# Kernel tuning notes

Measured on AMD Instinct MI355X. Metric: run time of the kernel, lower is better.

## Reference

```python
import jax, jax.numpy as jnp
import numpy as np

A = 9          # num anchors per location
C = 256        # feature channels
H = W = 32     # feature map size
B = 1          # batch (module's squeeze_-based NMS implies batch=1)
N = A * H * W  # total proposals
IOU_THR = 0.9
EPS = 1e-5     # BatchNorm eps
NEG_SLOPE = 0.01  # LeakyReLU default


def setup_inputs() -> dict:
    key = jax.random.key(0)
    ks = jax.random.split(key, 8)
    inp = {
        "x": jax.random.normal(ks[0], (B, C, H, W), dtype=jnp.float32),
        "anchors": jax.random.uniform(ks[1], (A, 4), dtype=jnp.float32),
        # depthwise 3x3 conv (groups=C): torch weight shape [C,1,3,3]
        "dw_w": jax.random.normal(ks[2], (C, 1, 3, 3), dtype=jnp.float32) * 0.05,
        # pointwise 1x1 conv [C_out, C_in]
        "pw_w": jax.random.normal(ks[3], (C, C), dtype=jnp.float32) * 0.05,
        "bn1_gamma": jnp.ones((C,), jnp.float32),
        "bn1_beta": jnp.zeros((C,), jnp.float32),
        "bn1_mean": jnp.zeros((C,), jnp.float32),
        "bn1_var": jnp.ones((C,), jnp.float32),
        # anchors_conv: 1x1 conv 256 -> 4A, BN, ReLU6
        "anc_w": jax.random.normal(ks[4], (4 * A, C), dtype=jnp.float32) * 0.05,
        "anc_gamma": jnp.ones((4 * A,), jnp.float32),
        "anc_beta": jnp.zeros((4 * A,), jnp.float32),
        "anc_mean": jnp.zeros((4 * A,), jnp.float32),
        "anc_var": jnp.ones((4 * A,), jnp.float32),
        # objectness_conv: 1x1 conv 256 -> A, BN, Sigmoid
        "obj_w": jax.random.normal(ks[5], (A, C), dtype=jnp.float32) * 0.05,
        "obj_gamma": jnp.ones((A,), jnp.float32),
        "obj_beta": jnp.zeros((A,), jnp.float32),
        "obj_mean": jnp.zeros((A,), jnp.float32),
        "obj_var": jnp.ones((A,), jnp.float32),
    }
    return inp


def _bn(h, gamma, beta, mean, var):
    # inference-mode BatchNorm2d over channel dim 1 of [B,C,H,W]
    inv = jax.lax.rsqrt(var + EPS)
    return (h - mean[None, :, None, None]) * (inv * gamma)[None, :, None, None] + beta[None, :, None, None]


def _nms_keep(boxes, scores, thr):
    # greedy NMS (torchvision semantics, boxes as x1,y1,x2,y2) -> bool keep mask in original order
    order = jnp.argsort(-scores)
    b = boxes[order]  # [N,4] sorted by score desc
    x1, y1, x2, y2 = b[:, 0], b[:, 1], b[:, 2], b[:, 3]
    areas = (x2 - x1) * (y2 - y1)
    ix1 = jnp.maximum(x1[:, None], x1[None, :])
    iy1 = jnp.maximum(y1[:, None], y1[None, :])
    ix2 = jnp.minimum(x2[:, None], x2[None, :])
    iy2 = jnp.minimum(y2[:, None], y2[None, :])
    inter = jnp.clip(ix2 - ix1, 0.0) * jnp.clip(iy2 - iy1, 0.0)
    iou = inter / (areas[:, None] + areas[None, :] - inter)
    idx = jnp.arange(boxes.shape[0])

    def body(i, keep):
        sup = (iou[i] > thr) & (idx > i) & keep[i]
        return keep & ~sup

    keep_sorted = jax.lax.fori_loop(0, boxes.shape[0], body, jnp.ones((boxes.shape[0],), bool))
    return jnp.zeros((boxes.shape[0],), bool).at[order].set(keep_sorted)


def reference(x, anchors, dw_w, pw_w, bn1_gamma, bn1_beta, bn1_mean, bn1_var,
              anc_w, anc_gamma, anc_beta, anc_mean, anc_var,
              obj_w, obj_gamma, obj_beta, obj_mean, obj_var):
    batch = x.shape[0]
    hw = x.shape[2] * x.shape[3]
    # DepthSeparableConv2d: depthwise 3x3 (groups=C) + pointwise 1x1
    h = jax.lax.conv_general_dilated(
        x, dw_w, window_strides=(1, 1), padding=((1, 1), (1, 1)),
        dimension_numbers=("NCHW", "OIHW", "NCHW"), feature_group_count=C)
    h = jnp.einsum("bchw,oc->bohw", h, pw_w)
    h = jax.nn.leaky_relu(_bn(h, bn1_gamma, bn1_beta, bn1_mean, bn1_var), NEG_SLOPE)
    # heads
    anc = jnp.einsum("bchw,oc->bohw", h, anc_w)
    anc = jnp.clip(_bn(anc, anc_gamma, anc_beta, anc_mean, anc_var), 0.0, 6.0)  # ReLU6
    obj = jnp.einsum("bchw,oc->bohw", h, obj_w)
    obj = jax.nn.sigmoid(_bn(obj, obj_gamma, obj_beta, obj_mean, obj_var))
    # anchor decode
    corr = anc.reshape(batch, A, 4, hw)              # [B,A,4,HW]
    anch = anchors.reshape(1, A, 4, 1)
    pos = corr[:, :, :2, :] + anch[:, :, :2, :]
    size = jnp.exp(corr[:, :, 2:, :]) * anch[:, :, 2:, :]
    corrected = jnp.concatenate([pos, size], axis=2)  # [B,A,4,HW]
    boxes = corrected.transpose(0, 2, 1, 3).reshape(batch, 4, -1).transpose(0, 2, 1)  # [B,N,4]
    scores = obj.reshape(batch, A, 1, hw).transpose(0, 2, 1, 3).reshape(batch, 1, -1).transpose(0, 2, 1)  # [B,N,1]
    boxes = boxes[0]          # squeeze_ (batch==1)
    scores = scores[0, :, 0]
    keep = _nms_keep(boxes, scores, IOU_THR)
    m = jax.lax.stop_gradient(keep.astype(boxes.dtype))
    # fixed-shape equivalent of index_select: suppressed rows zeroed
    return jnp.concatenate([boxes * m[:, None], (scores * m)[:, None]], axis=1)  # [N,5]
```

## Files before the change

### kernel.cpp

```cpp
#include <hip/hip_runtime.h>
#include <hip/hip_bf16.h>

#define EPSF 1e-5f
#define IOU_THRF 0.9f
#define NBOX 9216
#define NWORDS 144
#define CAND_CAP 4096
#define FIRE_CAP 1024
#define NTILES 666

__global__ __launch_bounds__(256) void dw_conv(const float* __restrict__ x,
                                               const float* __restrict__ w,
                                               float* __restrict__ h0) {
    int idx = blockIdx.x * 256 + threadIdx.x;
    int c = idx >> 10, p = idx & 1023;
    int yy = p >> 5, xx = p & 31;
    const float* xi = x + (c << 10);
    const float* wc = w + c * 9;
    float acc = 0.f;
    #pragma unroll
    for (int dy = -1; dy <= 1; ++dy) {
        int y2 = yy + dy;
        if ((unsigned)y2 >= 32u) continue;
        #pragma unroll
        for (int dx = -1; dx <= 1; ++dx) {
            int x2 = xx + dx;
            if ((unsigned)x2 >= 32u) continue;
            acc += wc[(dy + 1) * 3 + (dx + 1)] * xi[y2 * 32 + x2];
        }
    }
    h0[idx] = acc;
}

__global__ __launch_bounds__(256) void pw_conv(const float* __restrict__ h0,
                                               const float* __restrict__ w,
                                               const float* __restrict__ g,
                                               const float* __restrict__ b,
                                               const float* __restrict__ mu,
                                               const float* __restrict__ var,
                                               float* __restrict__ h1) {
    int p = blockIdx.x * 256 + threadIdx.x;
    int o0 = blockIdx.y * 4;
    float acc0 = 0.f, acc1 = 0.f, acc2 = 0.f, acc3 = 0.f;
    for (int c = 0; c < 256; ++c) {
        float hv = h0[(c << 10) + p];
        acc0 += w[(o0 + 0) * 256 + c] * hv;
        acc1 += w[(o0 + 1) * 256 + c] * hv;
        acc2 += w[(o0 + 2) * 256 + c] * hv;
        acc3 += w[(o0 + 3) * 256 + c] * hv;
    }
    float accs[4] = {acc0, acc1, acc2, acc3};
    #pragma unroll
    for (int k = 0; k < 4; ++k) {
        int o = o0 + k;
        float inv = 1.0f / sqrtf(var[o] + EPSF);
        float v = (accs[k] - mu[o]) * (inv * g[o]) + b[o];
        v = (v >= 0.f) ? v : 0.01f * v;
        h1[(o << 10) + p] = v;
    }
}

__global__ __launch_bounds__(256) void heads(const float* __restrict__ h1,
                                             const float* __restrict__ anc_w,
                                             const float* __restrict__ ag,
                                             const float* __restrict__ ab,
                                             const float* __restrict__ am,
                                             const float* __restrict__ av,
                                             const float* __restrict__ obj_w,
                                             const float* __restrict__ og,
                                             const float* __restrict__ ob,
                                             const float* __restrict__ om,
                                             const float* __restrict__ ov,
                                             const float* __restrict__ anchors,
                                             float* __restrict__ boxes,
                                             float* __restrict__ scores) {
    int p = blockIdx.x * 256 + threadIdx.x;
    int o = blockIdx.y;
    const float* wrow = (o < 36) ? (anc_w + o * 256) : (obj_w + (o - 36) * 256);
    float acc = 0.f;
    for (int c = 0; c < 256; ++c) acc += wrow[c] * h1[(c << 10) + p];
    if (o < 36) {
        float inv = 1.0f / sqrtf(av[o] + EPSF);
        float v = (acc - am[o]) * (inv * ag[o]) + ab[o];
        v = fminf(fmaxf(v, 0.f), 6.f);
        int a = o >> 2, k = o & 3;
        float anch = anchors[a * 4 + k];
        float val = (k < 2) ? (v + anch) : (expf(v) * anch);
        boxes[(size_t)(a * 1024 + p) * 4 + k] = val;
    } else {
        int a = o - 36;
        float inv = 1.0f / sqrtf(ov[a] + EPSF);
        float v = (acc - om[a]) * (inv * og[a]) + ob[a];
        scores[a * 1024 + p] = 1.0f / (1.0f + expf(-v));
    }
}

__global__ __launch_bounds__(256) void rank_partial(const float* __restrict__ scores,
                                                    unsigned* __restrict__ rank) {
    __shared__ float4 sm[144];
    int mbase = blockIdx.y * 576;
    for (int t = threadIdx.x; t < 144; t += 256)
        sm[t] = ((const float4*)(scores + mbase))[t];
    __syncthreads();
    int n = blockIdx.x * 256 + threadIdx.x;
    float s = scores[n];
    unsigned cnt = 0;
    for (int q = 0; q < 144; ++q) {
        float4 v = sm[q];
        int m = mbase + q * 4;
        cnt += (v.x > s) || (v.x == s && (m + 0) < n);
        cnt += (v.y > s) || (v.y == s && (m + 1) < n);
        cnt += (v.z > s) || (v.z == s && (m + 2) < n);
        cnt += (v.w > s) || (v.w == s && (m + 3) < n);
    }
    atomicAdd(&rank[n], cnt);
}

__global__ __launch_bounds__(256) void scatter_sorted(const float* __restrict__ boxes,
                                                      const unsigned* __restrict__ rank,
                                                      int* __restrict__ order,
                                                      float* __restrict__ sboxes,
                                                      float* __restrict__ sareas) {
    int n = blockIdx.x * 256 + threadIdx.x;
    unsigned r = rank[n];
    order[r] = n;
    float4 bx = ((const float4*)boxes)[n];
    ((float4*)sboxes)[r] = bx;
    sareas[r] = (bx.z - bx.x) * (bx.w - bx.y);
}

__global__ __launch_bounds__(256) void cand_detect(const float* __restrict__ sboxes,
                                                   const float* __restrict__ sareas,
                                                   unsigned long long* __restrict__ rnz64) {
    __shared__ float CX1[256], CY1[256], CX2[256], CY2[256], CAR[256];
    int rem = blockIdx.x, rb = 0;
    while (rem >= 36 - rb) { rem -= 36 - rb; ++rb; }
    int s = rb + rem;
    int tid = threadIdx.x;
    int i = rb * 256 + tid;
    {
        int j = s * 256 + tid;
        float4 cb = ((const float4*)sboxes)[j];
        CX1[tid] = cb.x; CY1[tid] = cb.y; CX2[tid] = cb.z; CY2[tid] = cb.w;
        CAR[tid] = sareas[j];
    }
    __syncthreads();
    float4 b = ((const float4*)sboxes)[i];
    float ar = sareas[i];
    bool any = false;

    if (s == rb) {
        for (int idx = tid + 1; idx < 256; ++idx) {
            float ix = fminf(b.z, CX2[idx]) - fmaxf(b.x, CX1[idx]);
            float iy = fminf(b.w, CY2[idx]) - fmaxf(b.y, CY1[idx]);
            float inter = fmaxf(ix, 0.f) * fmaxf(iy, 0.f);
            float denom = ar + CAR[idx] - inter;
            if (inter > 0.85f * denom) {
                if (inter / denom > IOU_THRF) any = true;
            }
        }
    } else {
        const float4* X1v = (const float4*)CX1;
        const float4* Y1v = (const float4*)CY1;
        const float4* X2v = (const float4*)CX2;
        const float4* Y2v = (const float4*)CY2;
        const float4* ARv = (const float4*)CAR;
        #pragma unroll 2
        for (int q = 0; q < 64; ++q) {
            float4 x1 = X1v[q], y1 = Y1v[q], x2 = X2v[q], y2 = Y2v[q], aa = ARv[q];
            #define CCHK(k) { \
                float ix = fminf(b.z, x2.k) - fmaxf(b.x, x1.k); \
                float iy = fminf(b.w, y2.k) - fmaxf(b.y, y1.k); \
                float inter = fmaxf(ix, 0.f) * fmaxf(iy, 0.f);  \
                float denom = ar + aa.k - inter;                \
                if (inter > 0.85f * denom) {                    \
                    if (inter / denom > IOU_THRF) any = true;   \
                } }
            CCHK(x) CCHK(y) CCHK(z) CCHK(w)
            #undef CCHK
        }
    }
    unsigned long long bal = __ballot(any);
    if ((tid & 63) == 0) atomicOr(&rnz64[rb * 4 + (tid >> 6)], bal);
}

__device__ inline unsigned long long rdl64(unsigned long long v, int l) {
    unsigned lo = (unsigned)__builtin_amdgcn_readlane((int)(unsigned)(v & 0xffffffffull), l);
    unsigned hi = (unsigned)__builtin_amdgcn_readlane((int)(unsigned)(v >> 32), l);
    return ((unsigned long long)hi << 32) | lo;
}

__global__ __launch_bounds__(64) void compact_cand(const unsigned long long* __restrict__ rnz64,
                                                   const float* __restrict__ sboxes,
                                                   const float* __restrict__ sareas,
                                                   int* __restrict__ cidx,
                                                   float4* __restrict__ cboxes,
                                                   float* __restrict__ carea,
                                                   int* __restrict__ knum) {
    int lane = threadIdx.x;
    unsigned long long rz0 = rnz64[lane];
    unsigned long long rz1 = rnz64[64 + lane];
    unsigned long long rz2 = rnz64[128 + lane];
    int base = 0;
    for (int w = 0; w < NWORDS; ++w) {
        unsigned long long bits = (w < 64) ? rdl64(rz0, w)
                                : (w < 128) ? rdl64(rz1, w - 64) : rdl64(rz2, w - 128);
        if (bits & (1ull << lane)) {
            int pos = base + (int)__popcll(bits & ((1ull << lane) - 1ull));
            if (pos < CAND_CAP) {
                int i = w * 64 + lane;
                cidx[pos] = i;
                cboxes[pos] = ((const float4*)sboxes)[i];
                carea[pos] = sareas[i];
            }
        }
        base += (int)__popcll(bits);
    }
    if (lane == 0) knum[0] = base < CAND_CAP ? base : CAND_CAP;
}

__global__ __launch_bounds__(256) void gate_build(const float4* __restrict__ cboxes,
                                                  const float* __restrict__ carea,
                                                  const int* __restrict__ knum,
                                                  unsigned long long* __restrict__ gate) {
    int Kc = knum[0];
    int a = blockIdx.x * 4 + (threadIdx.x >> 6);
    int w = threadIdx.x & 63;
    if (a >= Kc) return;
    float4 b = cboxes[a];
    float ar = carea[a];
    unsigned long long bits = 0ull;
    int cbase = w * 64;
    if (cbase < Kc) {
        int lim = Kc - cbase; if (lim > 64) lim = 64;
        for (int t = 0; t < lim; ++t) {
            int c = cbase + t;
            if (c > a) {
                float4 cb = cboxes[c];
                float ix = fminf(b.z, cb.z) - fmaxf(b.x, cb.x);
                float iy = fminf(b.w, cb.w) - fmaxf(b.y, cb.y);
                float inter = fmaxf(ix, 0.f) * fmaxf(iy, 0.f);
                float denom = ar + carea[c] - inter;
                if (inter > 0.85f * denom) {
                    if (inter / denom > IOU_THRF) bits |= (1ull << t);
                }
            }
        }
    }
    gate[(size_t)a * 64 + w] = bits;
}

__global__ __launch_bounds__(512) void nms_scan4(const unsigned long long* __restrict__ gate,
                                                 const int* __restrict__ knum,
                                                 int* __restrict__ fire_ord,
                                                 int* __restrict__ fire_cnt) {
    __shared__ unsigned long long tile[2][4096];
    int tid = threadIdx.x;
    int lane = tid & 63;
    int Kc = knum[0];
    int nw = (Kc + 63) >> 6;

    {
        const ulonglong2* src = (const ulonglong2*)gate;
        ulonglong2* dst = (ulonglong2*)tile[0];
        #pragma unroll
        for (int q = 0; q < 4; ++q) dst[tid + 512 * q] = src[tid + 512 * q];
    }
    __syncthreads();

    unsigned long long sup = 0ull;
    int nf = 0;

    for (int w = 0; w < nw; ++w) {
        int cur = w & 1, nxt = cur ^ 1;
        if (w + 1 < nw) {
            const ulonglong2* src = (const ulonglong2*)(gate + (size_t)(w + 1) * 4096);
            ulonglong2* dst = (ulonglong2*)tile[nxt];
            #pragma unroll
            for (int q = 0; q < 4; ++q) dst[tid + 512 * q] = src[tid + 512 * q];
        }
        if (tid < 64) {
            int rem = Kc - (w << 6);
            unsigned long long maskw = (rem >= 64) ? ~0ull : ((1ull << rem) - 1ull);
            unsigned long long alive = ~rdl64(sup, w) & maskw;
            while (alive) {
                int t = __builtin_ctzll(alive);
                if (lane == 0 && nf < FIRE_CAP) fire_ord[nf] = (w << 6) + t;
                ++nf;
                unsigned long long g = tile[cur][t * 64 + lane];
                sup |= g;
                alive &= ~(1ull << t);
                alive &= ~rdl64(g, w);
            }
        }
        __syncthreads();
    }
    if (tid == 0) fire_cnt[0] = nf < FIRE_CAP ? nf : FIRE_CAP;
}

__global__ __launch_bounds__(256) void finalize(const float* __restrict__ sboxes,
                                                const float* __restrict__ sareas,
                                                const float* __restrict__ scores,
                                                const int* __restrict__ order,
                                                const float4* __restrict__ cboxes,
                                                const float* __restrict__ carea,
                                                const int* __restrict__ cidx,
                                                const int* __restrict__ fire_ord,
                                                const int* __restrict__ fire_cnt,
                                                float* __restrict__ out) {
    __shared__ float4 FB[FIRE_CAP];
    __shared__ float FA[FIRE_CAP];
    __shared__ int FP[FIRE_CAP];
    int tid = threadIdx.x;
    int fc = fire_cnt[0];
    for (int k = tid; k < fc; k += 256) {
        int o = fire_ord[k];
        FB[k] = cboxes[o];
        FA[k] = carea[o];
        FP[k] = cidx[o];
    }
    __syncthreads();
    int j = blockIdx.x * 256 + tid;
    float4 b = ((const float4*)sboxes)[j];
    float aj = sareas[j];
    bool supp = false;
    for (int k = 0; k < fc; ++k) {
        float4 f = FB[k];
        float ix = fminf(b.z, f.z) - fmaxf(b.x, f.x);
        float iy = fminf(b.w, f.w) - fmaxf(b.y, f.y);
        float inter = fmaxf(ix, 0.f) * fmaxf(iy, 0.f);
        float denom = FA[k] + aj - inter;
        if (FP[k] < j && inter > 0.85f * denom) {
            if (inter / denom > IOU_THRF) supp = true;
        }
    }
    int n = order[j];
    float m = supp ? 0.f : 1.f;
    out[(size_t)n * 5 + 0] = b.x * m;
    out[(size_t)n * 5 + 1] = b.y * m;
    out[(size_t)n * 5 + 2] = b.z * m;
    out[(size_t)n * 5 + 3] = b.w * m;
    out[(size_t)n * 5 + 4] = scores[n] * m;
}

extern "C" void kernel_launch(void* const* d_in, const int* in_sizes, int n_in,
                              void* d_out, int out_size, void* d_ws, size_t ws_size,
                              hipStream_t stream) {
    const float* x      = (const float*)d_in[0];
    const float* anchors= (const float*)d_in[1];
    const float* dw_w   = (const float*)d_in[2];
    const float* pw_w   = (const float*)d_in[3];
    const float* bn1g   = (const float*)d_in[4];
    const float* bn1b   = (const float*)d_in[5];
    const float* bn1m   = (const float*)d_in[6];
    const float* bn1v   = (const float*)d_in[7];
    const float* anc_w  = (const float*)d_in[8];
    const float* ag     = (const float*)d_in[9];
    const float* ab     = (const float*)d_in[10];
    const float* am     = (const float*)d_in[11];
    const float* av     = (const float*)d_in[12];
    const float* obj_w  = (const float*)d_in[13];
    const float* og     = (const float*)d_in[14];
    const float* ob     = (const float*)d_in[15];
    const float* om     = (const float*)d_in[16];
    const float* ov     = (const float*)d_in[17];
    float* out = (float*)d_out;

    char* ws = (char*)d_ws;
    size_t off = 0;
    auto alloc = [&](size_t bytes) -> char* {
        char* p = ws + off;
        off = (off + bytes + 255) & ~(size_t)255;
        return p;
    };
    float* h0      = (float*)alloc(256 * 1024 * 4);
    float* h1      = (float*)alloc(256 * 1024 * 4);
    float* boxes   = (float*)alloc(NBOX * 4 * 4);
    float* scores  = (float*)alloc(NBOX * 4);
    unsigned* rank = (unsigned*)alloc(NBOX * 4);
    int* order     = (int*)alloc(NBOX * 4);
    float* sboxes  = (float*)alloc(NBOX * 4 * 4);
    float* sareas  = (float*)alloc(NBOX * 4);
    unsigned long long* rnz64 = (unsigned long long*)alloc(192 * 8);
    int* cidx      = (int*)alloc(CAND_CAP * 4);
    float4* cboxes = (float4*)alloc(CAND_CAP * 16);
    float* carea   = (float*)alloc(CAND_CAP * 4);
    int* knum      = (int*)alloc(256);
    int* fire_ord  = (int*)alloc(FIRE_CAP * 4);
    int* fire_cnt  = (int*)alloc(256);
    unsigned long long* gate = (unsigned long long*)alloc((size_t)CAND_CAP * 64 * 8);

    hipMemsetAsync(rank, 0, NBOX * 4, stream);
    hipMemsetAsync(rnz64, 0, 192 * 8, stream);

    dw_conv<<<1024, 256, 0, stream>>>(x, dw_w, h0);
    pw_conv<<<dim3(4, 64), 256, 0, stream>>>(h0, pw_w, bn1g, bn1b, bn1m, bn1v, h1);
    heads<<<dim3(4, 45), 256, 0, stream>>>(h1, anc_w, ag, ab, am, av,
                                           obj_w, og, ob, om, ov, anchors, boxes, scores);
    rank_partial<<<dim3(36, 16), 256, 0, stream>>>(scores, rank);
    scatter_sorted<<<36, 256, 0, stream>>>(boxes, rank, order, sboxes, sareas);
    cand_detect<<<NTILES, 256, 0, stream>>>(sboxes, sareas, rnz64);
    compact_cand<<<1, 64, 0, stream>>>(rnz64, sboxes, sareas, cidx, cboxes, carea, knum);
    gate_build<<<CAND_CAP / 4, 256, 0, stream>>>(cboxes, carea, knum, gate);
    nms_scan4<<<1, 512, 0, stream>>>(gate, knum, fire_ord, fire_cnt);
    finalize<<<36, 256, 0, stream>>>(sboxes, sareas, scores, order,
                                     cboxes, carea, cidx, fire_ord, fire_cnt, out);
}
```

Measured before the change: 369.3 us.

## Restructure serial NMS scan with diagonal gate words and lagged suppression OR

gate_build now also writes, for each candidate, its suppression word for its own 64-block (diag0) and for the next block (diag1). The single-block scan keeps only these diagonal words in LDS. The wave-0 greedy loop resolves each 64-candidate word using diag0 and carries diag1 into the next word. The other seven waves meanwhile atomically OR the full gate rows of the previous word's fired boxes into a shared suppression vector. This replaces streaming the whole 32KB gate tile into LDS for every word with sparse row reads that overlap the serial scan. In exchange it uses LDS atomics and relies on a one-word lag being correct.

```diff
diff --git a/kernel.cpp b/kernel.cpp
--- a/kernel.cpp
+++ b/kernel.cpp
@@ -222,7 +222,9 @@
 __global__ __launch_bounds__(256) void gate_build(const float4* __restrict__ cboxes,
                                                   const float* __restrict__ carea,
                                                   const int* __restrict__ knum,
-                                                  unsigned long long* __restrict__ gate) {
+                                                  unsigned long long* __restrict__ gate,
+                                                  unsigned long long* __restrict__ diag0,
+                                                  unsigned long long* __restrict__ diag1) {
     int Kc = knum[0];
     int a = blockIdx.x * 4 + (threadIdx.x >> 6);
     int w = threadIdx.x & 63;
@@ -248,50 +250,72 @@
         }
     }
     gate[(size_t)a * 64 + w] = bits;
-}
-
-__global__ __launch_bounds__(512) void nms_scan4(const unsigned long long* __restrict__ gate,
+    int aw = a >> 6;
+    if (w == aw) diag0[a] = bits;
+    if (w == aw + 1) diag1[a] = bits;
+}
+
+__global__ __launch_bounds__(512) void nms_scan5(const unsigned long long* __restrict__ gate,
+                                                 const unsigned long long* __restrict__ diag0,
+                                                 const unsigned long long* __restrict__ diag1,
                                                  const int* __restrict__ knum,
                                                  int* __restrict__ fire_ord,
                                                  int* __restrict__ fire_cnt) {
-    __shared__ unsigned long long tile[2][4096];
+    __shared__ unsigned long long d0L[CAND_CAP];
+    __shared__ unsigned long long d1L[CAND_CAP];
+    __shared__ unsigned long long supL[64];
+    __shared__ int flist[2][64];
+    __shared__ int fcnt[2];
     int tid = threadIdx.x;
-    int lane = tid & 63;
     int Kc = knum[0];
     int nw = (Kc + 63) >> 6;
 
-    {
-        const ulonglong2* src = (const ulonglong2*)gate;
-        ulonglong2* dst = (ulonglong2*)tile[0];
-        #pragma unroll
-        for (int q = 0; q < 4; ++q) dst[tid + 512 * q] = src[tid + 512 * q];
-    }
+    #pragma unroll
+    for (int q = 0; q < CAND_CAP / 512; ++q) {
+        d0L[tid + 512 * q] = diag0[tid + 512 * q];
+        d1L[tid + 512 * q] = diag1[tid + 512 * q];
+    }
+    if (tid < 64) supL[tid] = 0ull;
+    if (tid == 0) { fcnt[0] = 0; fcnt[1] = 0; }
     __syncthreads();
 
-    unsigned long long sup = 0ull;
     int nf = 0;
+    unsigned long long carry = 0ull;
 
     for (int w = 0; w < nw; ++w) {
-        int cur = w & 1, nxt = cur ^ 1;
-        if (w + 1 < nw) {
-            const ulonglong2* src = (const ulonglong2*)(gate + (size_t)(w + 1) * 4096);
-            ulonglong2* dst = (ulonglong2*)tile[nxt];
-            #pragma unroll
-            for (int q = 0; q < 4; ++q) dst[tid + 512 * q] = src[tid + 512 * q];
-        }
-        if (tid < 64) {
+        if (tid >= 64) {
+            int wv = (tid >> 6) - 1;
+            int j = tid & 63;
+            int fp = fcnt[(w + 1) & 1];
+            for (int f = wv; f < fp; f += 7) {
+                int o = flist[(w + 1) & 1][f];
+                if (j < nw) {
+                    unsigned long long g = gate[(size_t)o * 64 + j];
+                    if (g) atomicOr(&supL[j], g);
+                }
+            }
+        } else {
             int rem = Kc - (w << 6);
             unsigned long long maskw = (rem >= 64) ? ~0ull : ((1ull << rem) - 1ull);
-            unsigned long long alive = ~rdl64(sup, w) & maskw;
+            unsigned long long alive = ~(supL[w] | carry) & maskw;
+            unsigned long long carry_next = 0ull;
+            int myf = 0;
             while (alive) {
                 int t = __builtin_ctzll(alive);
-                if (lane == 0 && nf < FIRE_CAP) fire_ord[nf] = (w << 6) + t;
-                ++nf;
-                unsigned long long g = tile[cur][t * 64 + lane];
-                sup |= g;
+                int o = (w << 6) + t;
+                if (tid == 0) {
+                    if (nf < FIRE_CAP) fire_ord[nf] = o;
+                    flist[w & 1][myf] = o;
+                }
+                ++nf; ++myf;
+                unsigned long long dd0 = d0L[o];
+                unsigned long long dd1 = d1L[o];
                 alive &= ~(1ull << t);
-                alive &= ~rdl64(g, w);
+                alive &= ~dd0;
+                carry_next |= dd1;
             }
+            if (tid == 0) fcnt[w & 1] = myf;
+            carry = carry_next;
         }
         __syncthreads();
     }
@@ -388,7 +412,9 @@
     int* knum      = (int*)alloc(256);
     int* fire_ord  = (int*)alloc(FIRE_CAP * 4);
     int* fire_cnt  = (int*)alloc(256);
-    unsigned long long* gate = (unsigned long long*)alloc((size_t)CAND_CAP * 64 * 8);
+    unsigned long long* gate  = (unsigned long long*)alloc((size_t)CAND_CAP * 64 * 8);
+    unsigned long long* diag0 = (unsigned long long*)alloc(CAND_CAP * 8);
+    unsigned long long* diag1 = (unsigned long long*)alloc(CAND_CAP * 8);
 
     hipMemsetAsync(rank, 0, NBOX * 4, stream);
     hipMemsetAsync(rnz64, 0, 192 * 8, stream);
@@ -401,8 +427,8 @@
     scatter_sorted<<<36, 256, 0, stream>>>(boxes, rank, order, sboxes, sareas);
     cand_detect<<<NTILES, 256, 0, stream>>>(sboxes, sareas, rnz64);
     compact_cand<<<1, 64, 0, stream>>>(rnz64, sboxes, sareas, cidx, cboxes, carea, knum);
-    gate_build<<<CAND_CAP / 4, 256, 0, stream>>>(cboxes, carea, knum, gate);
-    nms_scan4<<<1, 512, 0, stream>>>(gate, knum, fire_ord, fire_cnt);
+    gate_build<<<CAND_CAP / 4, 256, 0, stream>>>(cboxes, carea, knum, gate, diag0, diag1);
+    nms_scan5<<<1, 512, 0, stream>>>(gate, diag0, diag1, knum, fire_ord, fire_cnt);
     finalize<<<36, 256, 0, stream>>>(sboxes, sareas, scores, order,
                                      cboxes, carea, cidx, fire_ord, fire_cnt, out);
 }
```

Result: faster. 349.8 us (-5.3%).
